# Kernel optimization log

Hardware: AMD Instinct MI355X
Metric: run time of the kernel (lower is better)

The kernel has to match this reference:

```python
import jax, jax.numpy as jnp
import numpy as np

UNITS = 50257
CUTOFF = [2000, 10000, UNITS]  # _cutoff = cutoff + [units]
C = 1024                        # channels (d_model)
N = 4096                        # flattened tokens (batch*seq)
N_TAILS = len(CUTOFF) - 1       # 2
ROOT_OUT = CUTOFF[0] + N_TAILS  # 2002
TAIL_DIMS = [256, 64]           # round(C/4**(i+1)/8)*8


def setup_inputs() -> dict:
    key = jax.random.key(0)
    ks = jax.random.split(key, 7)
    logits = jax.random.normal(ks[0], (N, C), jnp.float32)
    targets = jax.random.randint(ks[1], (N,), 0, UNITS, jnp.int32)
    s = 0.02
    head_kernel = jax.random.normal(ks[2], (C, ROOT_OUT), jnp.float32) * s
    proj0 = jax.random.normal(ks[3], (C, TAIL_DIMS[0]), jnp.float32) * s
    scale0 = jax.random.normal(ks[4], (TAIL_DIMS[0], CUTOFF[1] - CUTOFF[0]), jnp.float32) * s
    proj1 = jax.random.normal(ks[5], (C, TAIL_DIMS[1]), jnp.float32) * s
    scale1 = jax.random.normal(ks[6], (TAIL_DIMS[1], CUTOFF[2] - CUTOFF[1]), jnp.float32) * s
    return {"logits": logits, "targets": targets, "head_kernel": head_kernel,
            "proj0": proj0, "scale0": scale0, "proj1": proj1, "scale1": scale1}


def _sparse_ce(lg, labels):
    # sparse softmax cross entropy, numerically stable (single logsumexp)
    lse = jax.nn.logsumexp(lg, axis=-1)
    picked = jnp.take_along_axis(lg, labels[:, None].astype(jnp.int32), axis=1)[:, 0]
    return lse - picked


def reference(logits, targets, head_kernel, proj0, scale0, proj1, scale1):
    # Faithful jax version of AdaptiveSoftmax._train_loss (return_probs=False,
    # dropout=0, no bias on Denses, loss_reduction=SUM_OVER_BATCH_SIZE i.e. mean).
    # Dynamic boolean gather is replaced by dense compute + masked mean, which
    # yields identical math under jit (mean over the routed subset).
    root_logits = (logits @ head_kernel).astype(jnp.float32)  # [N, ROOT_OUT]
    root_targets = targets
    tails = [(proj0, scale0), (proj1, scale1)]
    losses = []
    for i, (p, s) in enumerate(tails):
        lo, hi = CUTOFF[i], CUTOFF[i + 1]
        m = (targets >= lo) & (targets < hi)
        root_targets = jnp.where(m, CUTOFF[0] + i, root_targets)
        tail_logits = ((logits @ p) @ s).astype(jnp.float32)  # [N, hi-lo]
        tail_tgt = jnp.clip(targets - lo, 0, hi - lo - 1)
        ce = _sparse_ce(tail_logits, tail_tgt)
        mf = m.astype(jnp.float32)
        losses.append(jnp.sum(ce * mf) / jnp.maximum(jnp.sum(mf), 1.0))
    root_loss = jnp.mean(_sparse_ce(root_logits, root_targets))
    all_losses = jnp.stack([root_loss] + losses)
    return jnp.mean(all_losses)
```

## Files before the change

kernel.cpp:

```cpp
#include <hip/hip_runtime.h>
#include <math.h>
#include <stdint.h>

#define NROWS 4096
#define CDIM 1024
#define T0_LO 2000
#define T0_HI 10000
#define T1_LO 10000
#define ROOT_COLS 2002
#define ROOT_PAD 2048
#define T0_COLS 8000
#define T0_PAD 8064
#define T1_COLS 40257
#define T1_PAD 40320
#define HB_STRIDE 320
#define LOG2E 1.44269504088896340736f
#define LN2 0.69314718055994530942f

using short8  = __attribute__((ext_vector_type(8))) short;
using ushort8 = __attribute__((ext_vector_type(8))) unsigned short;
using floatx4 = __attribute__((ext_vector_type(4))) float;

__device__ __forceinline__ unsigned short f2bf(float x) {
  union { float f; unsigned int u; } v; v.f = x;
  unsigned int r = v.u + 0x7fffu + ((v.u >> 16) & 1u);
  return (unsigned short)(r >> 16);
}
__device__ __forceinline__ float bf2f(unsigned short h) {
  union { unsigned int u; float f; } v; v.u = ((unsigned int)h) << 16;
  return v.f;
}
__device__ __forceinline__ floatx4 mfma16(short8 a, short8 b, floatx4 c) {
  return __builtin_amdgcn_mfma_f32_16x16x32_bf16(a, b, c, 0, 0, 0);
}
__device__ __forceinline__ void stage16(const unsigned short* g,
                                        unsigned short* lds_wave_base, int lane) {
#if __has_builtin(__builtin_amdgcn_global_load_lds)
  __builtin_amdgcn_global_load_lds(
      (const __attribute__((address_space(1))) void*)g,
      (__attribute__((address_space(3))) void*)lds_wave_base, 16, 0, 0);
#else
  ((ushort8*)lds_wave_base)[lane] = *(const ushort8*)g;
#endif
}

static constexpr size_t B_HB  = 0;
static constexpr size_t B_LB  = B_HB + 4096ull * 320 * 2;
static constexpr size_t B_WP  = B_LB + 4096ull * 1024 * 2;
static constexpr size_t B_WH  = B_WP + 384ull * 1024 * 2;
static constexpr size_t B_WS0 = B_WH + 2048ull * 1024 * 2;
static constexpr size_t B_WS1 = B_WS0 + 8064ull * 256 * 2;
static constexpr size_t B_S   = B_WS1 + 40320ull * 64 * 2;
static constexpr size_t B_P   = B_S + 3ull * 4096 * 4;
static constexpr size_t B_I0  = B_P + 3ull * 4096 * 4;
static constexpr size_t B_I1  = B_I0 + 4096ull * 4;
static constexpr size_t B_CNT = B_I1 + 4096ull * 4;

#define PR_WH_END   2048
#define PR_WP0_END  (PR_WH_END + 256)
#define PR_WP1_END  (PR_WP0_END + 64)
#define PR_WS0_END  (PR_WP1_END + 2016)
#define PR_WS1_END  (PR_WS0_END + 2520)
#define PR_ZERO_END (PR_WS1_END + 32)
#define PR_LB_END   (PR_ZERO_END + 2048)
#define PR_S_END    (PR_LB_END + 4)
#define PR_TOTAL    (PR_S_END + 1)

__global__ __launch_bounds__(256) void prep_kernel(
    const float* __restrict__ head, const float* __restrict__ proj0,
    const float* __restrict__ proj1, const float* __restrict__ scale0,
    const float* __restrict__ scale1, const float* __restrict__ logits,
    const int* __restrict__ targets,
    unsigned short* __restrict__ Wh, unsigned short* __restrict__ Wp,
    unsigned short* __restrict__ Ws0, unsigned short* __restrict__ Ws1,
    unsigned short* __restrict__ Lb, float* __restrict__ S,
    int* __restrict__ idx0, int* __restrict__ idx1, int* __restrict__ cnt) {
  const int id = blockIdx.x, tid = threadIdx.x;
  if (id >= PR_S_END) {
    __shared__ int base[2];
    if (tid < 2) base[tid] = 0;
    __syncthreads();
    for (int n = tid; n < NROWS; n += 256) {
      int t = targets[n];
      if (t >= T0_LO && t < T0_HI) idx0[atomicAdd(&base[0], 1)] = n;
      else if (t >= T1_LO)         idx1[atomicAdd(&base[1], 1)] = n;
    }
    __syncthreads();
    if (tid < 2) cnt[tid] = base[tid];
    return;
  }
  if (id >= PR_LB_END) {
    int rel = id - PR_LB_END;
    float4 z = make_float4(0.f, 0.f, 0.f, 0.f);
#pragma unroll
    for (int j = 0; j < 3; j++)
      ((float4*)S)[rel * 768 + j * 256 + tid] = z;
    return;
  }
  if (id >= PR_ZERO_END) {
    size_t base = (size_t)(id - PR_ZERO_END) * 2048 + tid * 8;
    float4 v0 = *(const float4*)(logits + base);
    float4 v1 = *(const float4*)(logits + base + 4);
    ushort8 h;
    h[0] = f2bf(v0.x); h[1] = f2bf(v0.y); h[2] = f2bf(v0.z); h[3] = f2bf(v0.w);
    h[4] = f2bf(v1.x); h[5] = f2bf(v1.y); h[6] = f2bf(v1.z); h[7] = f2bf(v1.w);
    *(ushort8*)(Lb + base) = h;
    return;
  }
  if (id >= PR_WS1_END) {
    size_t off = (size_t)(id - PR_WS1_END) * 2048 + tid * 8;
    ushort8 z = {0, 0, 0, 0, 0, 0, 0, 0};
    *(ushort8*)(Wp + 320ull * 1024 + off) = z;
    return;
  }
  const float* W; unsigned short* Wt; int K, N, Npad, nx, rel; float scale;
  if (id < PR_WH_END)       { W = head;   Wt = Wh;  K = 1024; N = ROOT_COLS; Npad = ROOT_PAD; scale = LOG2E; nx = 64;   rel = id; }
  else if (id < PR_WP0_END) { W = proj0;  Wt = Wp;  K = 1024; N = 256;  Npad = 256;  scale = 1.f;  nx = 8;    rel = id - PR_WH_END; }
  else if (id < PR_WP1_END) { W = proj1;  Wt = Wp + 256 * 1024; K = 1024; N = 64; Npad = 64; scale = 1.f; nx = 2; rel = id - PR_WP0_END; }
  else if (id < PR_WS0_END) { W = scale0; Wt = Ws0; K = 256;  N = T0_COLS; Npad = T0_PAD; scale = LOG2E; nx = 252;  rel = id - PR_WP1_END; }
  else                      { W = scale1; Wt = Ws1; K = 64;   N = T1_COLS; Npad = T1_PAD; scale = LOG2E; nx = 1260; rel = id - PR_WS0_END; }
  __shared__ float tile[32][33];
  const int n0 = (rel % nx) * 32, k0 = (rel / nx) * 32;
  const int tx = tid & 31, ty = tid >> 5;
  for (int i = 0; i < 32; i += 8) {
    int k = k0 + ty + i, n = n0 + tx;
    tile[ty + i][tx] = (n < N) ? W[(size_t)k * N + n] * scale : 0.f;
  }
  __syncthreads();
  const int nloc = tid >> 3, kg = tid & 7;
  const int n = n0 + nloc;
  if (n < Npad) {
    union { unsigned short v[4]; uint2 u; } x;
#pragma unroll
    for (int j = 0; j < 4; j++) x.v[j] = f2bf(tile[kg * 4 + j][nloc]);
    *(uint2*)&Wt[(size_t)n * K + k0 + kg * 4] = x.u;
  }
}

template<int CI>
__device__ __forceinline__ void gemm64_kloop(
    unsigned short* A_lds,
    const unsigned short* Arow,
    const unsigned short* const (&Bbase)[CI],
    floatx4 (&acc)[CI][4], int tid) {
  const int lane = tid & 63, w = tid >> 6;
  const int m = lane & 15, quad = lane >> 4, keym = m & 7;
  int goff[4];
#pragma unroll
  for (int it = 0; it < 4; it++) {
    int s = w * 256 + it * 64 + lane;
    int r = s >> 4, p = s & 15;
    int cq = p ^ (r & 7);
    goff[it] = r * CDIM + cq * 8;
  }
#pragma unroll
  for (int it = 0; it < 4; it++)
    stage16(Arow + goff[it], &A_lds[(w * 256 + it * 64) * 8], lane);
  for (int h = 0; h < 8; h++) {
    unsigned short* cur = A_lds + (h & 1) * (64 * 128);
    unsigned short* nxt = A_lds + ((h + 1) & 1) * (64 * 128);
    __syncthreads();
    if (h + 1 < 8) {
#pragma unroll
      for (int it = 0; it < 4; it++)
        stage16(Arow + goff[it] + (h + 1) * 128,
                &nxt[(w * 256 + it * 64) * 8], lane);
    }
    short8 b[CI][4];
#pragma unroll
    for (int ci = 0; ci < CI; ci++)
#pragma unroll
      for (int ks = 0; ks < 4; ks++)
        b[ci][ks] = *(const short8*)(Bbase[ci] + h * 128 + ks * 32);
    short8 areg[4][4];
#pragma unroll
    for (int t = 0; t < 4; t++)
#pragma unroll
      for (int ks = 0; ks < 4; ks++) {
        int ch = ((ks << 2) + quad) ^ keym;
        areg[t][ks] = *(const short8*)&cur[(t * 16 + m) * 128 + (ch << 3)];
      }
#pragma unroll
    for (int ci = 0; ci < CI; ci++)
#pragma unroll
      for (int ks = 0; ks < 4; ks++)
#pragma unroll
        for (int t = 0; t < 4; t++)
          acc[ci][t] = mfma16(areg[t][ks], b[ci][ks], acc[ci][t]);
  }
}

__global__ __launch_bounds__(256) void gemm_hidden(
    const unsigned short* __restrict__ Lb,
    const unsigned short* __restrict__ Wp,
    unsigned short* __restrict__ Hb) {
  __shared__ unsigned short A_lds[64 * 256];
  const int tid = threadIdx.x;
  const int row0 = blockIdx.x * 64;
  const int cg0 = blockIdx.y;
  const int lane = tid & 63, w = tid >> 6;
  const int m = lane & 15, quad = lane >> 4;
  const floatx4 zf = {0.f, 0.f, 0.f, 0.f};
  floatx4 acc[1][4];
#pragma unroll
  for (int t = 0; t < 4; t++) acc[0][t] = zf;
  const unsigned short* Bb[1] = {
      Wp + (size_t)(cg0 * 64 + w * 16 + m) * CDIM + quad * 8};
  gemm64_kloop<1>(A_lds, Lb + (size_t)row0 * CDIM, Bb, acc, tid);
  int n = cg0 * 64 + w * 16 + m;
  if (n < HB_STRIDE) {
#pragma unroll
    for (int t = 0; t < 4; t++)
#pragma unroll
      for (int r = 0; r < 4; r++)
        Hb[(size_t)(row0 + t * 16 + quad * 4 + r) * HB_STRIDE + n] =
            f2bf(acc[0][t][r]);
  }
}

#define MG_ROOT 512
#define MG_T1   480
#define MG_T0   2688
#define MG_PICK 1024
#define MG_TOTAL (MG_ROOT + MG_T1 + MG_T0 + MG_PICK)

__device__ __forceinline__ void root_compute(
    const unsigned short* cur, const short8 (&b)[2][2], floatx4 (&acc)[2][8],
    int m, int quad, int keym) {
#pragma unroll
  for (int hf = 0; hf < 2; hf++) {
    short8 areg[4][2];
#pragma unroll
    for (int t = 0; t < 4; t++)
#pragma unroll
      for (int ks = 0; ks < 2; ks++) {
        int ch = ((ks << 2) + quad) ^ keym;
        areg[t][ks] = *(const short8*)&cur[(hf * 64 + t * 16 + m) * 64 + (ch << 3)];
      }
#pragma unroll
    for (int ci = 0; ci < 2; ci++)
#pragma unroll
      for (int ks = 0; ks < 2; ks++)
#pragma unroll
        for (int t = 0; t < 4; t++)
          acc[ci][hf * 4 + t] = mfma16(areg[t][ks], b[ci][ks], acc[ci][hf * 4 + t]);
  }
}

__device__ __forceinline__ void root_stage(
    const unsigned short* Arow, const int (&goff)[4], int koff,
    unsigned short* buf, int w, int lane) {
#pragma unroll
  for (int it = 0; it < 4; it++)
    stage16(Arow + goff[it] + koff, &buf[(it * 256 + w * 64) * 8], lane);
}

__device__ __forceinline__ void root_loadB(
    const unsigned short* const (&Bb)[2], int koff, short8 (&b)[2][2]) {
#pragma unroll
  for (int ci = 0; ci < 2; ci++)
#pragma unroll
    for (int ks = 0; ks < 2; ks++)
      b[ci][ks] = *(const short8*)(Bb[ci] + koff + ks * 32);
}

__device__ __forceinline__ void root_path(
    unsigned char* smem, int bx, int by,
    const unsigned short* __restrict__ Lb,
    const unsigned short* __restrict__ Wh, float* __restrict__ S) {
  unsigned short* bufA = (unsigned short*)smem;
  unsigned short* bufB = bufA + 128 * 64;
  const int tid = threadIdx.x;
  const int row0 = bx * 128;
  const int cg0 = by * 2;
  const int lane = tid & 63, w = tid >> 6;
  const int m = lane & 15, quad = lane >> 4, keym = m & 7;
  const floatx4 zf = {0.f, 0.f, 0.f, 0.f};
  floatx4 acc[2][8];
#pragma unroll
  for (int ci = 0; ci < 2; ci++)
#pragma unroll
    for (int t = 0; t < 8; t++) acc[ci][t] = zf;
  const unsigned short* Bb[2] = {
      Wh + (size_t)((cg0 + 0) * 64 + w * 16 + m) * CDIM + quad * 8,
      Wh + (size_t)((cg0 + 1) * 64 + w * 16 + m) * CDIM + quad * 8};
  const unsigned short* Arow = Lb + (size_t)row0 * CDIM;
  int goff[4];
#pragma unroll
  for (int it = 0; it < 4; it++) {
    int s = it * 256 + w * 64 + lane;
    int r = s >> 3, p = s & 7;
    int cq = p ^ (r & 7);
    goff[it] = r * CDIM + cq * 8;
  }
  short8 b0[2][2], b1[2][2];
  root_stage(Arow, goff, 0, bufA, w, lane);
  root_loadB(Bb, 0, b0);
  for (int hh = 0; hh < 8; hh++) {
    __syncthreads();
    root_stage(Arow, goff, (hh * 2 + 1) * 64, bufB, w, lane);
    root_loadB(Bb, (hh * 2 + 1) * 64, b1);
    root_compute(bufA, b0, acc, m, quad, keym);
    __syncthreads();
    if (hh < 7) {
      root_stage(Arow, goff, (hh * 2 + 2) * 64, bufA, w, lane);
      root_loadB(Bb, (hh * 2 + 2) * 64, b0);
    }
    root_compute(bufB, b1, acc, m, quad, keym);
  }
  __syncthreads();
  float* sums = (float*)smem;
  if (tid < 128) sums[tid] = 0.f;
  __syncthreads();
#pragma unroll
  for (int t = 0; t < 8; t++)
#pragma unroll
    for (int r = 0; r < 4; r++) {
      float e = __builtin_amdgcn_exp2f(acc[0][t][r]) +
                __builtin_amdgcn_exp2f(acc[1][t][r]);
      e += __shfl_xor(e, 1); e += __shfl_xor(e, 2);
      e += __shfl_xor(e, 4); e += __shfl_xor(e, 8);
      if (m == 0)
        atomicAdd(&sums[(t >> 2) * 64 + (t & 3) * 16 + quad * 4 + r], e);
    }
  __syncthreads();
  if (tid < 128) atomicAdd(&S[row0 + tid], sums[tid]);
}

template<int K, int TILES, int MODE>
__device__ __forceinline__ void tail_path(
    unsigned char* smem, int bx, int by,
    const unsigned short* __restrict__ Hb, int acol0,
    const unsigned short* __restrict__ Wt, int ncgpb,
    const int* __restrict__ idx, const int* __restrict__ cnt,
    float* __restrict__ S) {
  constexpr int BM = TILES * 16;
  constexpr int CpR = K / 8;
  constexpr int KS = K / 32;
  unsigned short* A_lds = (unsigned short*)smem;
  int* row_lds = (int*)(smem + (size_t)BM * K * 2);
  float* sum_lds = (float*)(smem + (size_t)BM * K * 2 + BM * 4);
  const int tid = threadIdx.x;
  const int count = cnt[MODE - 1];
  const int row0 = bx * BM;
  if (row0 >= count) return;
  if (tid < BM) {
    int r = row0 + tid;
    row_lds[tid] = (r < count) ? idx[r] : -1;
    sum_lds[tid] = 0.f;
  }
  __syncthreads();
#pragma unroll
  for (int i = 0; i < BM * CpR / 256; i++) {
    int c = tid + 256 * i;
    int rl = c / CpR, cq = c % CpR;
    int row = row_lds[rl];
    ushort8 v = {0, 0, 0, 0, 0, 0, 0, 0};
    if (row >= 0) v = *(const ushort8*)(Hb + (size_t)row * HB_STRIDE + acol0 + cq * 8);
    *(ushort8*)&A_lds[rl * K + ((cq ^ (rl & 7)) << 3)] = v;
  }
  __syncthreads();
  const int lane = tid & 63, w = tid >> 6;
  const int m = lane & 15, quad = lane >> 4, keym = m & 7;
  const floatx4 zf = {0.f, 0.f, 0.f, 0.f};
  short8 areg[TILES][KS];
#pragma unroll
  for (int t = 0; t < TILES; t++)
#pragma unroll
    for (int ks = 0; ks < KS; ks++) {
      int ch = ((ks << 2) + quad) ^ keym;
      areg[t][ks] = *(const short8*)&A_lds[(t * 16 + m) * K + (ch << 3)];
    }
  float runsum[TILES][4];
#pragma unroll
  for (int t = 0; t < TILES; t++)
#pragma unroll
    for (int r = 0; r < 4; r++) runsum[t][r] = 0.f;

  const int cg0 = by * ncgpb;
  const unsigned short* Bp = Wt + (size_t)(cg0 * 64 + w * 16 + m) * K + quad * 8;
  short8 b0[KS], b1[KS];
#pragma unroll
  for (int ks = 0; ks < KS; ks++) b0[ks] = *(const short8*)(Bp + ks * 32);
#pragma unroll
  for (int ks = 0; ks < KS; ks++)
    b1[ks] = *(const short8*)(Bp + (size_t)64 * K + ks * 32);

  for (int cc = 0; cc < ncgpb; cc += 2) {
    floatx4 acc[TILES];
#pragma unroll
    for (int t = 0; t < TILES; t++) acc[t] = zf;
#pragma unroll
    for (int ks = 0; ks < KS; ks++)
#pragma unroll
      for (int t = 0; t < TILES; t++) acc[t] = mfma16(areg[t][ks], b0[ks], acc[t]);
    if (cc + 2 < ncgpb) {
      const unsigned short* p = Bp + (size_t)(cc + 2) * 64 * K;
#pragma unroll
      for (int ks = 0; ks < KS; ks++) b0[ks] = *(const short8*)(p + ks * 32);
    }
#pragma unroll
    for (int t = 0; t < TILES; t++)
#pragma unroll
      for (int r = 0; r < 4; r++)
        runsum[t][r] += __builtin_amdgcn_exp2f(acc[t][r]);

#pragma unroll
    for (int t = 0; t < TILES; t++) acc[t] = zf;
#pragma unroll
    for (int ks = 0; ks < KS; ks++)
#pragma unroll
      for (int t = 0; t < TILES; t++) acc[t] = mfma16(areg[t][ks], b1[ks], acc[t]);
    if (cc + 3 < ncgpb) {
      const unsigned short* p = Bp + (size_t)(cc + 3) * 64 * K;
#pragma unroll
      for (int ks = 0; ks < KS; ks++) b1[ks] = *(const short8*)(p + ks * 32);
    }
#pragma unroll
    for (int t = 0; t < TILES; t++)
#pragma unroll
      for (int r = 0; r < 4; r++)
        runsum[t][r] += __builtin_amdgcn_exp2f(acc[t][r]);
  }

#pragma unroll
  for (int t = 0; t < TILES; t++)
#pragma unroll
    for (int r = 0; r < 4; r++) {
      float e = runsum[t][r];
      e += __shfl_xor(e, 1); e += __shfl_xor(e, 2);
      e += __shfl_xor(e, 4); e += __shfl_xor(e, 8);
      if (m == 0) atomicAdd(&sum_lds[t * 16 + quad * 4 + r], e);
    }
  __syncthreads();
  if (tid < BM) {
    int row = row_lds[tid];
    if (row >= 0) atomicAdd(&S[row], sum_lds[tid]);
  }
}

__device__ __forceinline__ void picked_path(
    int rel, const float* __restrict__ logits, const int* __restrict__ targets,
    const unsigned short* __restrict__ Wh,
    const unsigned short* __restrict__ Ws0,
    const unsigned short* __restrict__ Ws1,
    const unsigned short* __restrict__ Hb, float* __restrict__ P) {
  const int tid = threadIdx.x, lane = tid & 63;
  const int row = rel * 4 + (tid >> 6);
  const int t = targets[row];
  const int tr = (t >= T0_LO && t < T0_HI) ? T0_LO : ((t >= T1_LO) ? T0_LO + 1 : t);
  const float* a = logits + (size_t)row * CDIM + lane * 16;
  const unsigned short* wr = Wh + (size_t)tr * CDIM + lane * 16;
  float acc = 0.f;
#pragma unroll
  for (int q = 0; q < 2; q++) {
    ushort8 wv = *(const ushort8*)(wr + q * 8);
    float4 a0 = ((const float4*)a)[q * 2];
    float4 a1 = ((const float4*)a)[q * 2 + 1];
    acc += a0.x * bf2f(wv[0]) + a0.y * bf2f(wv[1]) + a0.z * bf2f(wv[2]) + a0.w * bf2f(wv[3]);
    acc += a1.x * bf2f(wv[4]) + a1.y * bf2f(wv[5]) + a1.z * bf2f(wv[6]) + a1.w * bf2f(wv[7]);
  }
#pragma unroll
  for (int off = 1; off < 64; off <<= 1) acc += __shfl_xor(acc, off);
  if (lane == 0) P[row] = acc * LN2;
  if (t >= T0_LO) {
    float acc2 = 0.f;
    if (t < T0_HI) {
      const unsigned short* h = Hb + (size_t)row * HB_STRIDE + lane * 4;
      const unsigned short* w2 = Ws0 + (size_t)(t - T0_LO) * 256 + lane * 4;
#pragma unroll
      for (int j = 0; j < 4; j++) acc2 += bf2f(h[j]) * bf2f(w2[j]);
    } else {
      acc2 = bf2f(Hb[(size_t)row * HB_STRIDE + 256 + lane]) *
             bf2f(Ws1[(size_t)(t - T1_LO) * 64 + lane]);
    }
#pragma unroll
    for (int off = 1; off < 64; off <<= 1) acc2 += __shfl_xor(acc2, off);
    if (lane == 0) P[(t < T0_HI ? NROWS : 2 * NROWS) + row] = acc2 * LN2;
  }
}

__global__ __launch_bounds__(256, 2) void mega_kernel(
    const unsigned short* __restrict__ Lb,
    const unsigned short* __restrict__ Wh,
    const unsigned short* __restrict__ Ws0,
    const unsigned short* __restrict__ Ws1,
    const unsigned short* __restrict__ Hb,
    const float* __restrict__ logits, const int* __restrict__ targets,
    const int* __restrict__ idx0, const int* __restrict__ idx1,
    const int* __restrict__ cnt, float* __restrict__ S, float* __restrict__ P) {
  __shared__ __align__(16) unsigned char smem[32768];
  int bid = blockIdx.x;
  if (bid < MG_ROOT) {
    int wk = ((bid & 7) << 6) + (bid >> 3);
    root_path(smem, wk >> 4, wk & 15, Lb, Wh, S);
    return;
  }
  bid -= MG_ROOT;
  if (bid < MG_T1) {
    int wk = (bid & 7) * 60 + (bid >> 3);
    tail_path<64, 8, 2>(smem, wk & 31, wk >> 5, Hb, 256, Ws1, 42, idx1, cnt,
                        S + 2 * NROWS);
    return;
  }
  bid -= MG_T1;
  if (bid < MG_T0) {
    int wk = (bid & 7) * 336 + (bid >> 3);
    tail_path<256, 2, 1>(smem, wk & 127, wk >> 7, Hb, 0, Ws0, 6, idx0, cnt,
                         S + NROWS);
    return;
  }
  bid -= MG_T0;
  picked_path(bid, logits, targets, Wh, Ws0, Ws1, Hb, P);
}

__global__ __launch_bounds__(1024) void loss_kernel(
    const int* __restrict__ targets,
    const float* __restrict__ S,
    const float* __restrict__ P,
    float* __restrict__ out) {
  const int tid = threadIdx.x;
  float sr = 0.f, s0 = 0.f, s1 = 0.f, c0 = 0.f, c1 = 0.f;
  for (int n = tid; n < NROWS; n += 1024) {
    int t = targets[n];
    sr += logf(S[n] - 46.f) - P[n];
    if (t >= T0_LO && t < T0_HI) { s0 += logf(S[NROWS + n] - 64.f) - P[NROWS + n]; c0 += 1.f; }
    else if (t >= T1_LO)         { s1 += logf(S[2 * NROWS + n] - 63.f) - P[2 * NROWS + n]; c1 += 1.f; }
  }
  for (int off = 32; off > 0; off >>= 1) {
    sr += __shfl_down(sr, off);
    s0 += __shfl_down(s0, off);
    s1 += __shfl_down(s1, off);
    c0 += __shfl_down(c0, off);
    c1 += __shfl_down(c1, off);
  }
  __shared__ float red[16][5];
  int wv = tid >> 6;
  if ((tid & 63) == 0) { red[wv][0] = sr; red[wv][1] = s0; red[wv][2] = s1; red[wv][3] = c0; red[wv][4] = c1; }
  __syncthreads();
  if (tid == 0) {
    sr = 0.f; s0 = 0.f; s1 = 0.f; c0 = 0.f; c1 = 0.f;
#pragma unroll
    for (int i = 0; i < 16; i++) {
      sr += red[i][0]; s0 += red[i][1]; s1 += red[i][2];
      c0 += red[i][3]; c1 += red[i][4];
    }
    float root_loss = sr / (float)NROWS;
    float l0 = s0 / fmaxf(c0, 1.f);
    float l1 = s1 / fmaxf(c1, 1.f);
    out[0] = (root_loss + l0 + l1) / 3.f;
  }
}

extern "C" void kernel_launch(void* const* d_in, const int* in_sizes, int n_in,
                              void* d_out, int out_size, void* d_ws, size_t ws_size,
                              hipStream_t stream) {
  const float* logits  = (const float*)d_in[0];
  const int*   targets = (const int*)d_in[1];
  const float* head    = (const float*)d_in[2];
  const float* proj0   = (const float*)d_in[3];
  const float* scale0  = (const float*)d_in[4];
  const float* proj1   = (const float*)d_in[5];
  const float* scale1  = (const float*)d_in[6];
  float* out = (float*)d_out;
  char* ws = (char*)d_ws;

  unsigned short* Hb  = (unsigned short*)(ws + B_HB);
  unsigned short* Lb  = (unsigned short*)(ws + B_LB);
  unsigned short* Wp  = (unsigned short*)(ws + B_WP);
  unsigned short* Wh  = (unsigned short*)(ws + B_WH);
  unsigned short* Ws0 = (unsigned short*)(ws + B_WS0);
  unsigned short* Ws1 = (unsigned short*)(ws + B_WS1);
  float* S = (float*)(ws + B_S);
  float* P = (float*)(ws + B_P);
  int* idx0 = (int*)(ws + B_I0);
  int* idx1 = (int*)(ws + B_I1);
  int* cnt  = (int*)(ws + B_CNT);

  prep_kernel<<<PR_TOTAL, 256, 0, stream>>>(head, proj0, proj1, scale0, scale1,
                                            logits, targets, Wh, Wp, Ws0, Ws1,
                                            Lb, S, idx0, idx1, cnt);
  gemm_hidden<<<dim3(64, 5), 256, 0, stream>>>(Lb, Wp, Hb);
  mega_kernel<<<MG_TOTAL, 256, 0, stream>>>(Lb, Wh, Ws0, Ws1, Hb, logits,
                                            targets, idx0, idx1, cnt, S, P);
  loss_kernel<<<1, 1024, 0, stream>>>(targets, S, P, out);
}
```

Measured before the change: 191.4 us.

## Overlap weight transposes with hidden GEMM and interleave mega-kernel block paths

The prep kernel is split in two. Only the logits cast, the projection transposes, the zeroing and the index build stay in the first kernel. The large head/scale weight transposes move into a new mid kernel that runs alongside the hidden-projection GEMM, so that work overlaps instead of serializing before it. The hidden GEMM blocks and the mega kernel's blocks get XCD-aware remapping, and the mega kernel interleaves root, tail and picked work across block IDs to balance load and L2 locality per XCD. The cost is more complex block-index arithmetic and a mid kernel that mixes heterogeneous work.

```diff
diff --git a/kernel.cpp b/kernel.cpp
--- a/kernel.cpp
+++ b/kernel.cpp
@@ -56,49 +56,44 @@
 static constexpr size_t B_I1  = B_I0 + 4096ull * 4;
 static constexpr size_t B_CNT = B_I1 + 4096ull * 4;
 
-#define PR_WH_END   2048
-#define PR_WP0_END  (PR_WH_END + 256)
-#define PR_WP1_END  (PR_WP0_END + 64)
-#define PR_WS0_END  (PR_WP1_END + 2016)
-#define PR_WS1_END  (PR_WS0_END + 2520)
-#define PR_ZERO_END (PR_WS1_END + 32)
-#define PR_LB_END   (PR_ZERO_END + 2048)
-#define PR_S_END    (PR_LB_END + 4)
-#define PR_TOTAL    (PR_S_END + 1)
-
-__global__ __launch_bounds__(256) void prep_kernel(
-    const float* __restrict__ head, const float* __restrict__ proj0,
-    const float* __restrict__ proj1, const float* __restrict__ scale0,
-    const float* __restrict__ scale1, const float* __restrict__ logits,
-    const int* __restrict__ targets,
-    unsigned short* __restrict__ Wh, unsigned short* __restrict__ Wp,
-    unsigned short* __restrict__ Ws0, unsigned short* __restrict__ Ws1,
-    unsigned short* __restrict__ Lb, float* __restrict__ S,
-    int* __restrict__ idx0, int* __restrict__ idx1, int* __restrict__ cnt) {
+__device__ __forceinline__ void transpose_tile(
+    const float* __restrict__ W, unsigned short* __restrict__ Wt,
+    int K, int N, int Npad, int nx, int rel, float scale,
+    float (*tile)[33], int tid) {
+  const int n0 = (rel % nx) * 32, k0 = (rel / nx) * 32;
+  const int tx = tid & 31, ty = tid >> 5;
+  for (int i = 0; i < 32; i += 8) {
+    int k = k0 + ty + i, n = n0 + tx;
+    tile[ty + i][tx] = (n < N) ? W[(size_t)k * N + n] * scale : 0.f;
+  }
+  __syncthreads();
+  const int nloc = tid >> 3, kg = tid & 7;
+  const int n = n0 + nloc;
+  if (n < Npad) {
+    union { unsigned short v[4]; uint2 u; } x;
+#pragma unroll
+    for (int j = 0; j < 4; j++) x.v[j] = f2bf(tile[kg * 4 + j][nloc]);
+    *(uint2*)&Wt[(size_t)n * K + k0 + kg * 4] = x.u;
+  }
+}
+
+#define PA_LB_END   2048
+#define PA_WP0_END  (PA_LB_END + 256)
+#define PA_WP1_END  (PA_WP0_END + 64)
+#define PA_ZERO_END (PA_WP1_END + 32)
+#define PA_S_END    (PA_ZERO_END + 4)
+#define PA_TOTAL    (PA_S_END + 1)
+
+__global__ __launch_bounds__(256) void prep_a_kernel(
+    const float* __restrict__ proj0, const float* __restrict__ proj1,
+    const float* __restrict__ logits, const int* __restrict__ targets,
+    unsigned short* __restrict__ Wp, unsigned short* __restrict__ Lb,
+    float* __restrict__ S, int* __restrict__ idx0, int* __restrict__ idx1,
+    int* __restrict__ cnt) {
+  __shared__ float tile[32][33];
   const int id = blockIdx.x, tid = threadIdx.x;
-  if (id >= PR_S_END) {
-    __shared__ int base[2];
-    if (tid < 2) base[tid] = 0;
-    __syncthreads();
-    for (int n = tid; n < NROWS; n += 256) {
-      int t = targets[n];
-      if (t >= T0_LO && t < T0_HI) idx0[atomicAdd(&base[0], 1)] = n;
-      else if (t >= T1_LO)         idx1[atomicAdd(&base[1], 1)] = n;
-    }
-    __syncthreads();
-    if (tid < 2) cnt[tid] = base[tid];
-    return;
-  }
-  if (id >= PR_LB_END) {
-    int rel = id - PR_LB_END;
-    float4 z = make_float4(0.f, 0.f, 0.f, 0.f);
-#pragma unroll
-    for (int j = 0; j < 3; j++)
-      ((float4*)S)[rel * 768 + j * 256 + tid] = z;
-    return;
-  }
-  if (id >= PR_ZERO_END) {
-    size_t base = (size_t)(id - PR_ZERO_END) * 2048 + tid * 8;
+  if (id < PA_LB_END) {
+    size_t base = (size_t)id * 2048 + tid * 8;
     float4 v0 = *(const float4*)(logits + base);
     float4 v1 = *(const float4*)(logits + base + 4);
     ushort8 h;
@@ -107,34 +102,38 @@
     *(ushort8*)(Lb + base) = h;
     return;
   }
-  if (id >= PR_WS1_END) {
-    size_t off = (size_t)(id - PR_WS1_END) * 2048 + tid * 8;
+  if (id < PA_WP1_END) {
+    if (id < PA_WP0_END)
+      transpose_tile(proj0, Wp, 1024, 256, 256, 8, id - PA_LB_END, 1.f, tile, tid);
+    else
+      transpose_tile(proj1, Wp + 256 * 1024, 1024, 64, 64, 2, id - PA_WP0_END,
+                     1.f, tile, tid);
+    return;
+  }
+  if (id < PA_ZERO_END) {
+    size_t off = (size_t)(id - PA_WP1_END) * 2048 + tid * 8;
     ushort8 z = {0, 0, 0, 0, 0, 0, 0, 0};
     *(ushort8*)(Wp + 320ull * 1024 + off) = z;
     return;
   }
-  const float* W; unsigned short* Wt; int K, N, Npad, nx, rel; float scale;
-  if (id < PR_WH_END)       { W = head;   Wt = Wh;  K = 1024; N = ROOT_COLS; Npad = ROOT_PAD; scale = LOG2E; nx = 64;   rel = id; }
-  else if (id < PR_WP0_END) { W = proj0;  Wt = Wp;  K = 1024; N = 256;  Npad = 256;  scale = 1.f;  nx = 8;    rel = id - PR_WH_END; }
-  else if (id < PR_WP1_END) { W = proj1;  Wt = Wp + 256 * 1024; K = 1024; N = 64; Npad = 64; scale = 1.f; nx = 2; rel = id - PR_WP0_END; }
-  else if (id < PR_WS0_END) { W = scale0; Wt = Ws0; K = 256;  N = T0_COLS; Npad = T0_PAD; scale = LOG2E; nx = 252;  rel = id - PR_WP1_END; }
-  else                      { W = scale1; Wt = Ws1; K = 64;   N = T1_COLS; Npad = T1_PAD; scale = LOG2E; nx = 1260; rel = id - PR_WS0_END; }
-  __shared__ float tile[32][33];
-  const int n0 = (rel % nx) * 32, k0 = (rel / nx) * 32;
-  const int tx = tid & 31, ty = tid >> 5;
-  for (int i = 0; i < 32; i += 8) {
-    int k = k0 + ty + i, n = n0 + tx;
-    tile[ty + i][tx] = (n < N) ? W[(size_t)k * N + n] * scale : 0.f;
-  }
-  __syncthreads();
-  const int nloc = tid >> 3, kg = tid & 7;
-  const int n = n0 + nloc;
-  if (n < Npad) {
-    union { unsigned short v[4]; uint2 u; } x;
-#pragma unroll
-    for (int j = 0; j < 4; j++) x.v[j] = f2bf(tile[kg * 4 + j][nloc]);
-    *(uint2*)&Wt[(size_t)n * K + k0 + kg * 4] = x.u;
-  }
+  if (id < PA_S_END) {
+    int rel = id - PA_ZERO_END;
+    float4 z = make_float4(0.f, 0.f, 0.f, 0.f);
+#pragma unroll
+    for (int j = 0; j < 3; j++)
+      ((float4*)S)[rel * 768 + j * 256 + tid] = z;
+    return;
+  }
+  __shared__ int base2[2];
+  if (tid < 2) base2[tid] = 0;
+  __syncthreads();
+  for (int n = tid; n < NROWS; n += 256) {
+    int t = targets[n];
+    if (t >= T0_LO && t < T0_HI) idx0[atomicAdd(&base2[0], 1)] = n;
+    else if (t >= T1_LO)         idx1[atomicAdd(&base2[1], 1)] = n;
+  }
+  __syncthreads();
+  if (tid < 2) cnt[tid] = base2[tid];
 }
 
 template<int CI>
@@ -190,32 +189,50 @@
   }
 }
 
-__global__ __launch_bounds__(256) void gemm_hidden(
-    const unsigned short* __restrict__ Lb,
-    const unsigned short* __restrict__ Wp,
-    unsigned short* __restrict__ Hb) {
-  __shared__ unsigned short A_lds[64 * 256];
-  const int tid = threadIdx.x;
-  const int row0 = blockIdx.x * 64;
-  const int cg0 = blockIdx.y;
-  const int lane = tid & 63, w = tid >> 6;
-  const int m = lane & 15, quad = lane >> 4;
-  const floatx4 zf = {0.f, 0.f, 0.f, 0.f};
-  floatx4 acc[1][4];
-#pragma unroll
-  for (int t = 0; t < 4; t++) acc[0][t] = zf;
-  const unsigned short* Bb[1] = {
-      Wp + (size_t)(cg0 * 64 + w * 16 + m) * CDIM + quad * 8};
-  gemm64_kloop<1>(A_lds, Lb + (size_t)row0 * CDIM, Bb, acc, tid);
-  int n = cg0 * 64 + w * 16 + m;
-  if (n < HB_STRIDE) {
-#pragma unroll
-    for (int t = 0; t < 4; t++)
-#pragma unroll
-      for (int r = 0; r < 4; r++)
-        Hb[(size_t)(row0 + t * 16 + quad * 4 + r) * HB_STRIDE + n] =
-            f2bf(acc[0][t][r]);
-  }
+#define K2_HID      320
+#define K2_WH_END   (K2_HID + 2048)
+#define K2_WS0_END  (K2_WH_END + 2016)
+#define K2_TOTAL    (K2_WS0_END + 2520)
+
+__global__ __launch_bounds__(256) void mid_kernel(
+    const float* __restrict__ head, const float* __restrict__ scale0,
+    const float* __restrict__ scale1,
+    const unsigned short* __restrict__ Lb, const unsigned short* __restrict__ Wp,
+    unsigned short* __restrict__ Wh, unsigned short* __restrict__ Ws0,
+    unsigned short* __restrict__ Ws1, unsigned short* __restrict__ Hb) {
+  __shared__ __align__(16) unsigned char smem2[32768];
+  const int id = blockIdx.x, tid = threadIdx.x;
+  if (id < K2_HID) {
+    const int xcd = id & 7, k = id >> 3;
+    const int row0 = (xcd * 8 + (k & 7)) * 64;
+    const int cg0 = k >> 3;
+    unsigned short* A_lds = (unsigned short*)smem2;
+    const int lane = tid & 63, w = tid >> 6;
+    const int m = lane & 15, quad = lane >> 4;
+    const floatx4 zf = {0.f, 0.f, 0.f, 0.f};
+    floatx4 acc[1][4];
+#pragma unroll
+    for (int t = 0; t < 4; t++) acc[0][t] = zf;
+    const unsigned short* Bb[1] = {
+        Wp + (size_t)(cg0 * 64 + w * 16 + m) * CDIM + quad * 8};
+    gemm64_kloop<1>(A_lds, Lb + (size_t)row0 * CDIM, Bb, acc, tid);
+    int n = cg0 * 64 + w * 16 + m;
+    if (n < HB_STRIDE) {
+#pragma unroll
+      for (int t = 0; t < 4; t++)
+#pragma unroll
+        for (int r = 0; r < 4; r++)
+          Hb[(size_t)(row0 + t * 16 + quad * 4 + r) * HB_STRIDE + n] =
+              f2bf(acc[0][t][r]);
+    }
+    return;
+  }
+  const float* W; unsigned short* Wt; int K, N, Npad, nx, rel; float scale;
+  int t = id - K2_HID;
+  if (t < 2048)      { W = head;   Wt = Wh;  K = 1024; N = ROOT_COLS; Npad = ROOT_PAD; scale = LOG2E; nx = 64;   rel = t; }
+  else if (t < 4064) { W = scale0; Wt = Ws0; K = 256;  N = T0_COLS;   Npad = T0_PAD;   scale = LOG2E; nx = 252;  rel = t - 2048; }
+  else               { W = scale1; Wt = Ws1; K = 64;   N = T1_COLS;   Npad = T1_PAD;   scale = LOG2E; nx = 1260; rel = t - 4064; }
+  transpose_tile(W, Wt, K, N, Npad, nx, rel, scale, (float(*)[33])smem2, tid);
 }
 
 #define MG_ROOT 512
@@ -490,28 +507,33 @@
     const int* __restrict__ idx0, const int* __restrict__ idx1,
     const int* __restrict__ cnt, float* __restrict__ S, float* __restrict__ P) {
   __shared__ __align__(16) unsigned char smem[32768];
-  int bid = blockIdx.x;
-  if (bid < MG_ROOT) {
-    int wk = ((bid & 7) << 6) + (bid >> 3);
+  const int bid = blockIdx.x;
+  const int xcd = bid & 7, l = bid >> 3;
+  int path, k;
+  if (l < 576) {
+    int g = l / 9, r = l - g * 9;
+    if (r == 0)      { path = 0; k = g; }
+    else if (r == 1) { if (g < 60) { path = 1; k = g; }
+                       else        { path = 2; k = 320 + (g - 60); } }
+    else if (r <= 6) { path = 2; k = g * 5 + (r - 2); }
+    else             { path = 3; k = g * 2 + (r - 7); }
+  } else {
+    path = 2; k = 324 + (l - 576);
+  }
+  if (path == 0) {
+    int wk = xcd * 64 + k;
     root_path(smem, wk >> 4, wk & 15, Lb, Wh, S);
-    return;
-  }
-  bid -= MG_ROOT;
-  if (bid < MG_T1) {
-    int wk = (bid & 7) * 60 + (bid >> 3);
+  } else if (path == 1) {
+    int wk = xcd * 60 + k;
     tail_path<64, 8, 2>(smem, wk & 31, wk >> 5, Hb, 256, Ws1, 42, idx1, cnt,
                         S + 2 * NROWS);
-    return;
-  }
-  bid -= MG_T1;
-  if (bid < MG_T0) {
-    int wk = (bid & 7) * 336 + (bid >> 3);
+  } else if (path == 2) {
+    int wk = xcd * 336 + k;
     tail_path<256, 2, 1>(smem, wk & 127, wk >> 7, Hb, 0, Ws0, 6, idx0, cnt,
                          S + NROWS);
-    return;
-  }
-  bid -= MG_T0;
-  picked_path(bid, logits, targets, Wh, Ws0, Ws1, Hb, P);
+  } else {
+    picked_path(xcd * 128 + k, logits, targets, Wh, Ws0, Ws1, Hb, P);
+  }
 }
 
 __global__ __launch_bounds__(1024) void loss_kernel(
@@ -577,10 +599,10 @@
   int* idx1 = (int*)(ws + B_I1);
   int* cnt  = (int*)(ws + B_CNT);
 
-  prep_kernel<<<PR_TOTAL, 256, 0, stream>>>(head, proj0, proj1, scale0, scale1,
-                                            logits, targets, Wh, Wp, Ws0, Ws1,
-                                            Lb, S, idx0, idx1, cnt);
-  gemm_hidden<<<dim3(64, 5), 256, 0, stream>>>(Lb, Wp, Hb);
+  prep_a_kernel<<<PA_TOTAL, 256, 0, stream>>>(proj0, proj1, logits, targets,
+                                              Wp, Lb, S, idx0, idx1, cnt);
+  mid_kernel<<<K2_TOTAL, 256, 0, stream>>>(head, scale0, scale1, Lb, Wp,
+                                           Wh, Ws0, Ws1, Hb);
   mega_kernel<<<MG_TOTAL, 256, 0, stream>>>(Lb, Wh, Ws0, Ws1, Hb, logits,
                                             targets, idx0, idx1, cnt, S, P);
   loss_kernel<<<1, 1024, 0, stream>>>(targets, S, P, out);
```

New measurement: 202.8 us. +5.9%, slower.
